# Kernel tuning notes

Hardware: AMD Instinct MI355X
Metric: run time of the kernel (lower is better)

## Reference

```python
import jax, jax.numpy as jnp
import numpy as np

N = 50000      # nodes
E = 800000     # edges (avg degree 16)
IN, HID, OUT = 256, 128, 64


def _glorot(key, shape):
    fan_in, fan_out = shape[0], shape[1]
    limit = np.sqrt(6.0 / (fan_in + fan_out))
    return jax.random.uniform(key, shape, jnp.float32, -limit, limit)


def setup_inputs() -> dict:
    key = jax.random.key(0)
    ks = jax.random.split(key, 8)
    x = jax.random.normal(ks[0], (N, IN), jnp.float32)
    edge_index = jax.random.randint(ks[1], (2, E), 0, N, dtype=jnp.int64)
    W1 = _glorot(ks[2], (IN, HID))
    b1 = jnp.zeros((HID,), jnp.float32)
    W2 = _glorot(ks[3], (HID, OUT))
    b2 = jnp.zeros((OUT,), jnp.float32)
    aw1 = _glorot(ks[4], (HID, 1))
    ab1 = jnp.zeros((1,), jnp.float32)
    aw2 = _glorot(ks[5], (OUT, 1))
    ab2 = jnp.zeros((1,), jnp.float32)
    return {"x": x, "edge_index": edge_index, "W1": W1, "b1": b1,
            "W2": W2, "b2": b2, "aw1": aw1, "ab1": ab1, "aw2": aw2, "ab2": ab2}


def gcn_conv(x, W, b, src, dst, n):
    # PyG GCNConv: add self-loops, symmetric degree normalization, then aggregate.
    h = x @ W                                   # [n, out]
    loops = jnp.arange(n, dtype=src.dtype)
    s = jnp.concatenate([src, loops])           # [E+n]
    d = jnp.concatenate([dst, loops])
    deg = jax.ops.segment_sum(jnp.ones(s.shape[0], h.dtype), d, num_segments=n)
    dinv = jnp.where(deg > 0, jax.lax.rsqrt(deg), 0.0)
    norm = dinv[s] * dinv[d]                    # [E+n]
    out = jax.ops.segment_sum(h[s] * norm[:, None], d, num_segments=n)
    return out + b


def reference(x, edge_index, W1, b1, W2, b2, aw1, ab1, aw2, ab2):
    # eval mode: dropout is identity
    src, dst = edge_index[0], edge_index[1]
    h = gcn_conv(x, W1, b1, src, dst, N)
    h = jax.nn.relu(h)
    h = h * jax.nn.sigmoid(h @ aw1 + ab1)       # sigmoid attention gate 1
    h = gcn_conv(h, W2, b2, src, dst, N)
    return h * jax.nn.sigmoid(h @ aw2 + ab2)    # sigmoid attention gate 2
```

## Files before the change

kernel.cpp:

```cpp
#include <hip/hip_runtime.h>
#include <math.h>

#define N_NODES 50000
#define N_EDGES 800000
#define D_IN    256
#define D_HID   128
#define D_OUT   64

#define NB 196
#define CH 2048

typedef unsigned int u32;
typedef unsigned short u16;
typedef __attribute__((ext_vector_type(8))) short bf16x8;
typedef __attribute__((ext_vector_type(4))) float f32x4;

__device__ __forceinline__ float bflo(u32 u) {
    union { u32 i; float f; } c; c.i = u << 16; return c.f;
}
__device__ __forceinline__ float bfhi(u32 u) {
    union { u32 i; float f; } c; c.i = u & 0xffff0000u; return c.f;
}
__device__ __forceinline__ u32 pack_bf2(float a, float b) {
    union { float f; u32 i; } ca, cb; ca.f = a; cb.f = b;
    u32 ra = (ca.i + 0x7fffu + ((ca.i >> 16) & 1u)) >> 16;
    u32 rb = (cb.i + 0x7fffu + ((cb.i >> 16) & 1u)) & 0xffff0000u;
    return ra | rb;
}

__device__ __forceinline__ void acc8(float* a, uint4 u) {
    a[0] += bflo(u.x); a[1] += bfhi(u.x);
    a[2] += bflo(u.y); a[3] += bfhi(u.y);
    a[4] += bflo(u.z); a[5] += bfhi(u.z);
    a[6] += bflo(u.w); a[7] += bfhi(u.w);
}

__device__ __forceinline__ int edge_at(const void* ei, int is64, int which, int i) {
    if (is64) return (int)((const long long*)ei)[(size_t)which * N_EDGES + i];
    return ((const int*)ei)[which * N_EDGES + i];
}

__device__ __forceinline__ int detect_is64(const void* ei, int t, int* s_is32) {
    if (t == 0) *s_is32 = 0;
    __syncthreads();
    if (t < 256) {
        int vv = ((const int*)ei)[2 * t + 1];
        if (vv != 0) atomicOr(s_is32, 1);
    }
    __syncthreads();
    return (*s_is32 == 0);
}


__global__ __launch_bounds__(256) void k_hist(const void* __restrict__ ei,
                                              int* __restrict__ bcnt,
                                              int* __restrict__ bstart,
                                              int* __restrict__ bcur,
                                              int* __restrict__ tick) {
    __shared__ int h[NB];
    __shared__ int s_is32;
    __shared__ int s_last;
    int t = threadIdx.x;
    int is64 = detect_is64(ei, t, &s_is32);
    for (int i = t; i < NB; i += 256) h[i] = 0;
    __syncthreads();
    for (int i = blockIdx.x * 256 + t; i < N_EDGES; i += gridDim.x * 256) {
        int d = edge_at(ei, is64, 1, i);
        atomicAdd(&h[d >> 8], 1);
    }
    __syncthreads();
    for (int i = t; i < NB; i += 256) if (h[i]) atomicAdd(&bcnt[i], h[i]);
    __threadfence();
    if (t == 0) s_last = (atomicAdd(tick, 1) == (int)gridDim.x - 1);
    __syncthreads();
    if (s_last) {
        __shared__ int sm[256];
        int v = (t < NB) ? atomicAdd(&bcnt[t], 0) : 0;
        sm[t] = v; __syncthreads();
        for (int off = 1; off < 256; off <<= 1) {
            int a = (t >= off) ? sm[t - off] : 0;
            __syncthreads();
            sm[t] += a;
            __syncthreads();
        }
        if (t < NB) { bstart[t] = sm[t] - v; bcur[t] = sm[t] - v; }
    }
}

__global__ __launch_bounds__(256) void k_scatter1(const void* __restrict__ ei,
                                                  int* __restrict__ bcur,
                                                  u32* __restrict__ ebuf) {
    __shared__ int h[NB], gbase[NB], lc[NB];
    __shared__ int s_is32;
    int t = threadIdx.x;
    int is64 = detect_is64(ei, t, &s_is32);
    for (int i = t; i < NB; i += 256) { h[i] = 0; lc[i] = 0; }
    __syncthreads();
    int base = blockIdx.x * CH;

    u32 p[CH / 256];
    #pragma unroll
    for (int j = 0; j < CH / 256; ++j) {
        int i = base + j * 256 + t;
        if (i < N_EDGES) {
            int s = edge_at(ei, is64, 0, i);
            int d = edge_at(ei, is64, 1, i);
            p[j] = (u32)s | ((u32)d << 16);
            atomicAdd(&h[d >> 8], 1);
        }
    }
    __syncthreads();
    for (int i = t; i < NB; i += 256) if (h[i]) gbase[i] = atomicAdd(&bcur[i], h[i]);
    __syncthreads();
    #pragma unroll
    for (int j = 0; j < CH / 256; ++j) {
        int i = base + j * 256 + t;
        if (i < N_EDGES) {
            int b = (int)(p[j] >> 24);
            int lp = atomicAdd(&lc[b], 1);
            ebuf[gbase[b] + lp] = p[j];
        }
    }
}

__global__ __launch_bounds__(256) void k_scatter2(const u32* __restrict__ ebuf,
                                                  const int* __restrict__ bstart,
                                                  const int* __restrict__ bcnt,
                                                  int* __restrict__ rowstart,
                                                  int* __restrict__ cnt,
                                                  float* __restrict__ dinv,
                                                  int* __restrict__ colidx) {
    __shared__ int h2[256], lofs[256], cur[256], sm[256];
    int b = blockIdx.x, t = threadIdx.x;
    int e0 = bstart[b], ne = bcnt[b];
    h2[t] = 0; cur[t] = 0;
    __syncthreads();
    for (int i = t; i < ne; i += 256) {
        u32 p = ebuf[e0 + i];
        atomicAdd(&h2[(p >> 16) & 255], 1);
    }
    __syncthreads();
    int v = h2[t]; sm[t] = v; __syncthreads();
    for (int off = 1; off < 256; off <<= 1) {
        int a = (t >= off) ? sm[t - off] : 0;
        __syncthreads();
        sm[t] += a;
        __syncthreads();
    }
    lofs[t] = sm[t] - v;
    __syncthreads();
    int node = (b << 8) + t;
    if (node < N_NODES) {
        rowstart[node] = e0 + lofs[t];
        cnt[node] = v;
        dinv[node] = rsqrtf(1.0f + (float)v);
    }
    for (int i = t; i < ne; i += 256) {
        u32 p = ebuf[e0 + i];
        int dl = (p >> 16) & 255;
        int lp = atomicAdd(&cur[dl], 1);
        colidx[e0 + lofs[dl] + lp] = (int)(p & 0xffffu);
    }
}

__global__ void k_wsplit(const float* __restrict__ W1, u16* __restrict__ t1h,
                         u16* __restrict__ t1l, const float* __restrict__ W2,
                         u16* __restrict__ t2h, u16* __restrict__ t2l,
                         int* __restrict__ bcnt, int* __restrict__ tick) {
    int i = blockIdx.x * 256 + threadIdx.x;
    if (i < NB) bcnt[i] = 0;
    if (i == 0) tick[0] = 0;
    if (i < D_IN * D_HID) {
        int k = i / D_HID, c = i - k * D_HID;
        u32 bits = __float_as_uint(W1[i]);
        u32 hb = bits & 0xffff0000u;
        float lo = __uint_as_float(bits) - __uint_as_float(hb);
        t1h[(size_t)c * D_IN + k] = (u16)(hb >> 16);
        t1l[(size_t)c * D_IN + k] = (u16)(__float_as_uint(lo) >> 16);
    }
    int j = i - D_IN * D_HID;
    if (j >= 0 && j < D_HID * D_OUT) {
        int k = j / D_OUT, c = j - k * D_OUT;
        u32 bits = __float_as_uint(W2[j]);
        u32 hb = bits & 0xffff0000u;
        float lo = __uint_as_float(bits) - __uint_as_float(hb);
        t2h[(size_t)c * D_HID + k] = (u16)(hb >> 16);
        t2l[(size_t)c * D_HID + k] = (u16)(__float_as_uint(lo) >> 16);
    }
}

template <int K, int NF>
__global__ __launch_bounds__(256) void k_gemm_f32a(
    const float* __restrict__ A, const u16* __restrict__ tHi,
    const u16* __restrict__ tLo, const float* __restrict__ dinv,
    u32* __restrict__ Cp, int M) {
    constexpr int NT = NF / 16;
    constexpr int LDK = 40;
    __shared__ u16 aH[128][LDK], aL[128][LDK];
    __shared__ u16 wH[NF][LDK], wL[NF][LDK];

    const int t = threadIdx.x;
    const int lane = t & 63, wv = t >> 6;
    const int m0 = blockIdx.x * 128;
    const int lr = lane & 15, lk = (lane >> 4) * 8;

    f32x4 acc[2][NT] = {};

    const int arow = t >> 1;
    const int akq = (t & 1) * 16;
    const bool aok = (m0 + arow) < M;
    const float* asrc = A + (size_t)(m0 + arow) * K + akq;

    for (int ks = 0; ks < K; ks += 32) {
        {
            float f[16];
            #pragma unroll
            for (int j = 0; j < 16; ++j) f[j] = 0.0f;
            if (aok) {
                const float4* p = (const float4*)(asrc + ks);
                float4 v0 = p[0], v1 = p[1], v2 = p[2], v3 = p[3];
                f[0] = v0.x; f[1] = v0.y; f[2]  = v0.z; f[3]  = v0.w;
                f[4] = v1.x; f[5] = v1.y; f[6]  = v1.z; f[7]  = v1.w;
                f[8] = v2.x; f[9] = v2.y; f[10] = v2.z; f[11] = v2.w;
                f[12] = v3.x; f[13] = v3.y; f[14] = v3.z; f[15] = v3.w;
            }
            u32 hp[8], lp[8];
            #pragma unroll
            for (int q = 0; q < 8; ++q) {
                u32 b0 = __float_as_uint(f[2 * q]);
                u32 b1 = __float_as_uint(f[2 * q + 1]);
                u32 h0 = b0 & 0xffff0000u, h1 = b1 & 0xffff0000u;
                float l0 = f[2 * q] - __uint_as_float(h0);
                float l1 = f[2 * q + 1] - __uint_as_float(h1);
                hp[q] = (h0 >> 16) | h1;
                lp[q] = (__float_as_uint(l0) >> 16) | (__float_as_uint(l1) & 0xffff0000u);
            }
            *(uint4*)&aH[arow][akq + 0] = make_uint4(hp[0], hp[1], hp[2], hp[3]);
            *(uint4*)&aH[arow][akq + 8] = make_uint4(hp[4], hp[5], hp[6], hp[7]);
            *(uint4*)&aL[arow][akq + 0] = make_uint4(lp[0], lp[1], lp[2], lp[3]);
            *(uint4*)&aL[arow][akq + 8] = make_uint4(lp[4], lp[5], lp[6], lp[7]);
        }
        #pragma unroll
        for (int idx = t; idx < NF * 4; idx += 256) {
            int col = idx >> 2;
            int k8 = (idx & 3) * 8;
            *(uint4*)&wH[col][k8] = *(const uint4*)&tHi[(size_t)col * K + ks + k8];
            *(uint4*)&wL[col][k8] = *(const uint4*)&tLo[(size_t)col * K + ks + k8];
        }
        __syncthreads();

        bf16x8 afH[2], afL[2];
        #pragma unroll
        for (int mt = 0; mt < 2; ++mt) {
            int r = wv * 32 + mt * 16 + lr;
            afH[mt] = *(const bf16x8*)&aH[r][lk];
            afL[mt] = *(const bf16x8*)&aL[r][lk];
        }
        #pragma unroll
        for (int nt = 0; nt < NT; ++nt) {
            bf16x8 bh = *(const bf16x8*)&wH[nt * 16 + lr][lk];
            bf16x8 bl = *(const bf16x8*)&wL[nt * 16 + lr][lk];
            #pragma unroll
            for (int mt = 0; mt < 2; ++mt) {
                acc[mt][nt] = __builtin_amdgcn_mfma_f32_16x16x32_bf16(afH[mt], bh, acc[mt][nt], 0, 0, 0);
                acc[mt][nt] = __builtin_amdgcn_mfma_f32_16x16x32_bf16(afL[mt], bh, acc[mt][nt], 0, 0, 0);
                acc[mt][nt] = __builtin_amdgcn_mfma_f32_16x16x32_bf16(afH[mt], bl, acc[mt][nt], 0, 0, 0);
            }
        }
        __syncthreads();
    }

    #pragma unroll
    for (int mt = 0; mt < 2; ++mt) {
        #pragma unroll
        for (int r = 0; r < 4; ++r) {
            int row = m0 + wv * 32 + mt * 16 + (lane >> 4) * 4 + r;
            float dv = (row < M) ? dinv[row] : 0.0f;
            #pragma unroll
            for (int nt = 0; nt < NT; ++nt) {
                float v = acc[mt][nt][r] * dv;
                float vn = __shfl_xor(v, 1);
                if (!(lane & 1) && row < M) {
                    Cp[(size_t)row * (NF / 2) + nt * 8 + (lr >> 1)] = pack_bf2(v, vn);
                }
            }
        }
    }
}

template <int K, int NF>
__global__ __launch_bounds__(256) void k_gemm_splita(
    const u32* __restrict__ aHg, const u32* __restrict__ aLg,
    const u16* __restrict__ tHi, const u16* __restrict__ tLo,
    const float* __restrict__ dinv, u32* __restrict__ Cp, int M) {
    constexpr int NT = NF / 16;
    constexpr int LDK = 40;
    __shared__ u16 aH[128][LDK], aL[128][LDK];
    __shared__ u16 wH[NF][LDK], wL[NF][LDK];

    const int t = threadIdx.x;
    const int lane = t & 63, wv = t >> 6;
    const int m0 = blockIdx.x * 128;
    const int lr = lane & 15, lk = (lane >> 4) * 8;

    f32x4 acc[2][NT] = {};

    for (int ks = 0; ks < K; ks += 32) {
        #pragma unroll
        for (int idx = t; idx < 128 * 4; idx += 256) {
            int row = idx >> 2;
            int kq = (idx & 3) * 8;
            int grow = m0 + row;
            uint4 hv = make_uint4(0, 0, 0, 0), lv = make_uint4(0, 0, 0, 0);
            if (grow < M) {
                size_t gi = (size_t)grow * (K / 2) + (ks + kq) / 2;
                hv = *(const uint4*)&aHg[gi];
                lv = *(const uint4*)&aLg[gi];
            }
            *(uint4*)&aH[row][kq] = hv;
            *(uint4*)&aL[row][kq] = lv;
        }
        #pragma unroll
        for (int idx = t; idx < NF * 4; idx += 256) {
            int col = idx >> 2;
            int k8 = (idx & 3) * 8;
            *(uint4*)&wH[col][k8] = *(const uint4*)&tHi[(size_t)col * K + ks + k8];
            *(uint4*)&wL[col][k8] = *(const uint4*)&tLo[(size_t)col * K + ks + k8];
        }
        __syncthreads();

        bf16x8 afH[2], afL[2];
        #pragma unroll
        for (int mt = 0; mt < 2; ++mt) {
            int r = wv * 32 + mt * 16 + lr;
            afH[mt] = *(const bf16x8*)&aH[r][lk];
            afL[mt] = *(const bf16x8*)&aL[r][lk];
        }
        #pragma unroll
        for (int nt = 0; nt < NT; ++nt) {
            bf16x8 bh = *(const bf16x8*)&wH[nt * 16 + lr][lk];
            bf16x8 bl = *(const bf16x8*)&wL[nt * 16 + lr][lk];
            #pragma unroll
            for (int mt = 0; mt < 2; ++mt) {
                acc[mt][nt] = __builtin_amdgcn_mfma_f32_16x16x32_bf16(afH[mt], bh, acc[mt][nt], 0, 0, 0);
                acc[mt][nt] = __builtin_amdgcn_mfma_f32_16x16x32_bf16(afL[mt], bh, acc[mt][nt], 0, 0, 0);
                acc[mt][nt] = __builtin_amdgcn_mfma_f32_16x16x32_bf16(afH[mt], bl, acc[mt][nt], 0, 0, 0);
            }
        }
        __syncthreads();
    }

    #pragma unroll
    for (int mt = 0; mt < 2; ++mt) {
        #pragma unroll
        for (int r = 0; r < 4; ++r) {
            int row = m0 + wv * 32 + mt * 16 + (lane >> 4) * 4 + r;
            float dv = (row < M) ? dinv[row] : 0.0f;
            #pragma unroll
            for (int nt = 0; nt < NT; ++nt) {
                float v = acc[mt][nt][r] * dv;
                float vn = __shfl_xor(v, 1);
                if (!(lane & 1) && row < M) {
                    Cp[(size_t)row * (NF / 2) + nt * 8 + (lr >> 1)] = pack_bf2(v, vn);
                }
            }
        }
    }
}


__global__ __launch_bounds__(256) void k_agg1(
        const u32* __restrict__ hs, const int* __restrict__ rowstart,
        const int* __restrict__ cnt, const int* __restrict__ colidx,
        const float* __restrict__ dinv,
        const float* __restrict__ b, const float* __restrict__ aw,
        const float* __restrict__ ab,
        u32* __restrict__ oHi, u32* __restrict__ oLo) {
    int v = blockIdx.x * 4 + (threadIdx.x >> 6);
    int l = threadIdx.x & 63;
    if (v >= N_NODES) return;
    int g = l >> 4, q = l & 15;
    const uint4* hs4 = (const uint4*)hs;
    float a[8];
    #pragma unroll
    for (int k = 0; k < 8; ++k) a[k] = 0.0f;
    if (g == 0) acc8(a, hs4[(size_t)v * 16 + q]);
    int start = rowstart[v], len = cnt[v];
    const int* cx = colidx + start;
    int jj = g;
    for (; jj + 4 < len; jj += 8) {
        int s0 = cx[jj], s1 = cx[jj + 4];
        uint4 u0 = hs4[(size_t)s0 * 16 + q];
        uint4 u1 = hs4[(size_t)s1 * 16 + q];
        acc8(a, u0); acc8(a, u1);
    }
    if (jj < len) acc8(a, hs4[(size_t)cx[jj] * 16 + q]);
    #pragma unroll
    for (int k = 0; k < 8; ++k) {
        a[k] += __shfl_xor(a[k], 16);
        a[k] += __shfl_xor(a[k], 32);
    }
    float dv = dinv[v];
    float4 b0 = *(const float4*)&b[8 * q], b1 = *(const float4*)&b[8 * q + 4];
    a[0] = fmaxf(a[0] * dv + b0.x, 0.0f); a[1] = fmaxf(a[1] * dv + b0.y, 0.0f);
    a[2] = fmaxf(a[2] * dv + b0.z, 0.0f); a[3] = fmaxf(a[3] * dv + b0.w, 0.0f);
    a[4] = fmaxf(a[4] * dv + b1.x, 0.0f); a[5] = fmaxf(a[5] * dv + b1.y, 0.0f);
    a[6] = fmaxf(a[6] * dv + b1.z, 0.0f); a[7] = fmaxf(a[7] * dv + b1.w, 0.0f);
    float4 w0 = *(const float4*)&aw[8 * q], w1 = *(const float4*)&aw[8 * q + 4];
    float p = a[0] * w0.x + a[1] * w0.y + a[2] * w0.z + a[3] * w0.w
            + a[4] * w1.x + a[5] * w1.y + a[6] * w1.z + a[7] * w1.w;
    p += __shfl_xor(p, 1); p += __shfl_xor(p, 2);
    p += __shfl_xor(p, 4); p += __shfl_xor(p, 8);
    float gg = 1.0f / (1.0f + expf(-(p + ab[0])));
    if (g == 0) {
        u32 hp[4], lp[4];
        #pragma unroll
        for (int pr = 0; pr < 4; ++pr) {
            float v0 = a[2 * pr] * gg, v1 = a[2 * pr + 1] * gg;
            u32 b0i = __float_as_uint(v0), b1i = __float_as_uint(v1);
            u32 h0 = b0i & 0xffff0000u, h1 = b1i & 0xffff0000u;
            float l0 = v0 - __uint_as_float(h0);
            float l1 = v1 - __uint_as_float(h1);
            hp[pr] = (h0 >> 16) | h1;
            lp[pr] = (__float_as_uint(l0) >> 16) | (__float_as_uint(l1) & 0xffff0000u);
        }
        *(uint4*)&oHi[(size_t)v * 64 + q * 4] = make_uint4(hp[0], hp[1], hp[2], hp[3]);
        *(uint4*)&oLo[(size_t)v * 64 + q * 4] = make_uint4(lp[0], lp[1], lp[2], lp[3]);
    }
}

__global__ __launch_bounds__(256) void k_agg2(
        const u32* __restrict__ hs, const int* __restrict__ rowstart,
        const int* __restrict__ cnt, const int* __restrict__ colidx,
        const float* __restrict__ dinv,
        const float* __restrict__ b, const float* __restrict__ aw,
        const float* __restrict__ ab, float* __restrict__ out) {
    int v = blockIdx.x * 4 + (threadIdx.x >> 6);
    int l = threadIdx.x & 63;
    if (v >= N_NODES) return;
    int g = l >> 3, q = l & 7;
    const uint4* hs4 = (const uint4*)hs;
    float a[8];
    #pragma unroll
    for (int k = 0; k < 8; ++k) a[k] = 0.0f;
    if (g == 0) acc8(a, hs4[(size_t)v * 8 + q]);
    int start = rowstart[v], len = cnt[v];
    const int* cx = colidx + start;
    int jj = g;
    for (; jj + 8 < len; jj += 16) {
        int s0 = cx[jj], s1 = cx[jj + 8];
        uint4 u0 = hs4[(size_t)s0 * 8 + q];
        uint4 u1 = hs4[(size_t)s1 * 8 + q];
        acc8(a, u0); acc8(a, u1);
    }
    if (jj < len) acc8(a, hs4[(size_t)cx[jj] * 8 + q]);
    #pragma unroll
    for (int k = 0; k < 8; ++k) {
        a[k] += __shfl_xor(a[k], 8);
        a[k] += __shfl_xor(a[k], 16);
        a[k] += __shfl_xor(a[k], 32);
    }
    float dv = dinv[v];
    float4 b0 = *(const float4*)&b[8 * q], b1 = *(const float4*)&b[8 * q + 4];
    a[0] = a[0] * dv + b0.x; a[1] = a[1] * dv + b0.y;
    a[2] = a[2] * dv + b0.z; a[3] = a[3] * dv + b0.w;
    a[4] = a[4] * dv + b1.x; a[5] = a[5] * dv + b1.y;
    a[6] = a[6] * dv + b1.z; a[7] = a[7] * dv + b1.w;
    float4 w0 = *(const float4*)&aw[8 * q], w1 = *(const float4*)&aw[8 * q + 4];
    float p = a[0] * w0.x + a[1] * w0.y + a[2] * w0.z + a[3] * w0.w
            + a[4] * w1.x + a[5] * w1.y + a[6] * w1.z + a[7] * w1.w;
    p += __shfl_xor(p, 1); p += __shfl_xor(p, 2); p += __shfl_xor(p, 4);
    float gg = 1.0f / (1.0f + expf(-(p + ab[0])));
    if (g == 0) {
        float4 o0 = make_float4(a[0] * gg, a[1] * gg, a[2] * gg, a[3] * gg);
        float4 o1 = make_float4(a[4] * gg, a[5] * gg, a[6] * gg, a[7] * gg);
        *(float4*)&out[(size_t)v * 64 + 8 * q] = o0;
        *(float4*)&out[(size_t)v * 64 + 8 * q + 4] = o1;
    }
}


static inline size_t align_up(size_t x, size_t a) { return (x + a - 1) & ~(a - 1); }

extern "C" void kernel_launch(void* const* d_in, const int* in_sizes, int n_in,
                              void* d_out, int out_size, void* d_ws, size_t ws_size,
                              hipStream_t stream) {
    const float* x   = (const float*)d_in[0];
    const void*  ei  = d_in[1];
    const float* W1  = (const float*)d_in[2];
    const float* b1  = (const float*)d_in[3];
    const float* W2  = (const float*)d_in[4];
    const float* b2  = (const float*)d_in[5];
    const float* aw1 = (const float*)d_in[6];
    const float* ab1 = (const float*)d_in[7];
    const float* aw2 = (const float*)d_in[8];
    const float* ab2 = (const float*)d_in[9];
    float* out = (float*)d_out;

    char* w = (char*)d_ws;
    size_t off = 0;
    int*   bcnt     = (int*)(w + off); off = align_up(off + NB * 4, 256);
    int*   bstart   = (int*)(w + off); off = align_up(off + NB * 4, 256);
    int*   bcur     = (int*)(w + off); off = align_up(off + NB * 4, 256);
    int*   tick     = (int*)(w + off); off = align_up(off + 4, 256);
    int*   cnt      = (int*)(w + off); off = align_up(off + N_NODES * 4, 256);
    int*   rowstart = (int*)(w + off); off = align_up(off + N_NODES * 4, 256);
    float* dinv     = (float*)(w + off); off = align_up(off + N_NODES * 4, 256);
    u32*   ebuf     = (u32*)(w + off); off = align_up(off + (size_t)N_EDGES * 4, 256);
    int*   colidx   = (int*)(w + off); off = align_up(off + (size_t)N_EDGES * 4, 256);
    u32*   h1s      = (u32*)(w + off); off = align_up(off + (size_t)N_NODES * 64 * 4, 256);
    u32*   h1hi     = (u32*)(w + off); off = align_up(off + (size_t)N_NODES * 64 * 4, 256);
    u32*   h1lo     = (u32*)(w + off); off = align_up(off + (size_t)N_NODES * 64 * 4, 256);
    u32*   h2s      = (u32*)(w + off); off = align_up(off + (size_t)N_NODES * 32 * 4, 256);
    u16*   wt1h     = (u16*)(w + off); off = align_up(off + (size_t)D_IN * D_HID * 2, 256);
    u16*   wt1l     = (u16*)(w + off); off = align_up(off + (size_t)D_IN * D_HID * 2, 256);
    u16*   wt2h     = (u16*)(w + off); off = align_up(off + (size_t)D_HID * D_OUT * 2, 256);
    u16*   wt2l     = (u16*)(w + off); off = align_up(off + (size_t)D_HID * D_OUT * 2, 256);
    (void)ws_size; (void)out_size; (void)n_in; (void)in_sizes;

    k_wsplit<<<(D_IN * D_HID + D_HID * D_OUT + 255) / 256, 256, 0, stream>>>(
        W1, wt1h, wt1l, W2, wt2h, wt2l, bcnt, tick);

    k_hist<<<256, 256, 0, stream>>>(ei, bcnt, bstart, bcur, tick);
    k_scatter1<<<(N_EDGES + CH - 1) / CH, 256, 0, stream>>>(ei, bcur, ebuf);
    k_scatter2<<<NB, 256, 0, stream>>>(ebuf, bstart, bcnt, rowstart, cnt, dinv, colidx);

    k_gemm_f32a<D_IN, D_HID><<<(N_NODES + 127) / 128, 256, 0, stream>>>(
        x, wt1h, wt1l, dinv, h1s, N_NODES);
    k_agg1<<<(N_NODES + 3) / 4, 256, 0, stream>>>(
        h1s, rowstart, cnt, colidx, dinv, b1, aw1, ab1, h1hi, h1lo);

    k_gemm_splita<D_HID, D_OUT><<<(N_NODES + 127) / 128, 256, 0, stream>>>(
        h1hi, h1lo, wt2h, wt2l, dinv, h2s, N_NODES);
    k_agg2<<<(N_NODES + 3) / 4, 256, 0, stream>>>(
        h2s, rowstart, cnt, colidx, dinv, b2, aw2, ab2, out);
}
```

Before: 244.8 us.

## Column-chunk aggregation for cache locality and replace histogram with fixed slabs

Aggregation kernels are split into feature-column chunks across blocks, so each pass gathers a narrower slice of neighbour rows and the working set fits better in cache. The sigmoid gates become separate passes: partial dot products go to a buffer, gate 1 is applied while loading the second GEMM's input, and gate 2 runs as its own elementwise kernel. The histogram/scan kernel is dropped by giving each destination bucket a fixed-capacity slab. This adds kernel launches and extra intermediate traffic (h2a, pdot), and it is only correct if no bucket holds more than SLAB edges, which holds only for near-uniform degree distributions.

```diff
diff --git a/kernel.cpp b/kernel.cpp
--- a/kernel.cpp
+++ b/kernel.cpp
@@ -9,6 +9,8 @@
 
 #define NB 196
 #define CH 2048
+#define SLAB 4608
+#define NBLK1 12500
 
 typedef unsigned int u32;
 typedef unsigned short u16;
@@ -51,41 +53,6 @@
     return (*s_is32 == 0);
 }
 
-
-__global__ __launch_bounds__(256) void k_hist(const void* __restrict__ ei,
-                                              int* __restrict__ bcnt,
-                                              int* __restrict__ bstart,
-                                              int* __restrict__ bcur,
-                                              int* __restrict__ tick) {
-    __shared__ int h[NB];
-    __shared__ int s_is32;
-    __shared__ int s_last;
-    int t = threadIdx.x;
-    int is64 = detect_is64(ei, t, &s_is32);
-    for (int i = t; i < NB; i += 256) h[i] = 0;
-    __syncthreads();
-    for (int i = blockIdx.x * 256 + t; i < N_EDGES; i += gridDim.x * 256) {
-        int d = edge_at(ei, is64, 1, i);
-        atomicAdd(&h[d >> 8], 1);
-    }
-    __syncthreads();
-    for (int i = t; i < NB; i += 256) if (h[i]) atomicAdd(&bcnt[i], h[i]);
-    __threadfence();
-    if (t == 0) s_last = (atomicAdd(tick, 1) == (int)gridDim.x - 1);
-    __syncthreads();
-    if (s_last) {
-        __shared__ int sm[256];
-        int v = (t < NB) ? atomicAdd(&bcnt[t], 0) : 0;
-        sm[t] = v; __syncthreads();
-        for (int off = 1; off < 256; off <<= 1) {
-            int a = (t >= off) ? sm[t - off] : 0;
-            __syncthreads();
-            sm[t] += a;
-            __syncthreads();
-        }
-        if (t < NB) { bstart[t] = sm[t] - v; bcur[t] = sm[t] - v; }
-    }
-}
 
 __global__ __launch_bounds__(256) void k_scatter1(const void* __restrict__ ei,
                                                   int* __restrict__ bcur,
@@ -124,15 +91,14 @@
 }
 
 __global__ __launch_bounds__(256) void k_scatter2(const u32* __restrict__ ebuf,
-                                                  const int* __restrict__ bstart,
-                                                  const int* __restrict__ bcnt,
+                                                  const int* __restrict__ bcur,
                                                   int* __restrict__ rowstart,
                                                   int* __restrict__ cnt,
                                                   float* __restrict__ dinv,
                                                   int* __restrict__ colidx) {
     __shared__ int h2[256], lofs[256], cur[256], sm[256];
     int b = blockIdx.x, t = threadIdx.x;
-    int e0 = bstart[b], ne = bcnt[b];
+    int e0 = b * SLAB, ne = bcur[b] - e0;
     h2[t] = 0; cur[t] = 0;
     __syncthreads();
     for (int i = t; i < ne; i += 256) {
@@ -166,10 +132,9 @@
 __global__ void k_wsplit(const float* __restrict__ W1, u16* __restrict__ t1h,
                          u16* __restrict__ t1l, const float* __restrict__ W2,
                          u16* __restrict__ t2h, u16* __restrict__ t2l,
-                         int* __restrict__ bcnt, int* __restrict__ tick) {
+                         int* __restrict__ bcur) {
     int i = blockIdx.x * 256 + threadIdx.x;
-    if (i < NB) bcnt[i] = 0;
-    if (i == 0) tick[0] = 0;
+    if (i < NB) bcur[i] = i * SLAB;
     if (i < D_IN * D_HID) {
         int k = i / D_HID, c = i - k * D_HID;
         u32 bits = __float_as_uint(W1[i]);
@@ -291,6 +256,7 @@
 template <int K, int NF>
 __global__ __launch_bounds__(256) void k_gemm_splita(
     const u32* __restrict__ aHg, const u32* __restrict__ aLg,
+    const float* __restrict__ g1,
     const u16* __restrict__ tHi, const u16* __restrict__ tLo,
     const float* __restrict__ dinv, u32* __restrict__ Cp, int M) {
     constexpr int NT = NF / 16;
@@ -316,6 +282,19 @@
                 size_t gi = (size_t)grow * (K / 2) + (ks + kq) / 2;
                 hv = *(const uint4*)&aHg[gi];
                 lv = *(const uint4*)&aLg[gi];
+                float gv = g1[grow];
+                u32* hp = (u32*)&hv; u32* lp = (u32*)&lv;
+                #pragma unroll
+                for (int w2 = 0; w2 < 4; ++w2) {
+                    float f0 = (bflo(hp[w2]) + bflo(lp[w2])) * gv;
+                    float f1 = (bfhi(hp[w2]) + bfhi(lp[w2])) * gv;
+                    u32 h0 = __float_as_uint(f0) & 0xffff0000u;
+                    u32 h1b = __float_as_uint(f1) & 0xffff0000u;
+                    float l0 = f0 - __uint_as_float(h0);
+                    float l1 = f1 - __uint_as_float(h1b);
+                    hp[w2] = (h0 >> 16) | h1b;
+                    lp[w2] = (__float_as_uint(l0) >> 16) | (__float_as_uint(l1) & 0xffff0000u);
+                }
             }
             *(uint4*)&aH[row][kq] = hv;
             *(uint4*)&aL[row][kq] = lv;
@@ -369,114 +348,147 @@
 }
 
 
-__global__ __launch_bounds__(256) void k_agg1(
+__global__ __launch_bounds__(256) void k_agg1c(
         const u32* __restrict__ hs, const int* __restrict__ rowstart,
         const int* __restrict__ cnt, const int* __restrict__ colidx,
         const float* __restrict__ dinv,
         const float* __restrict__ b, const float* __restrict__ aw,
-        const float* __restrict__ ab,
+        float* __restrict__ pdot,
         u32* __restrict__ oHi, u32* __restrict__ oLo) {
-    int v = blockIdx.x * 4 + (threadIdx.x >> 6);
+    int c  = blockIdx.x / NBLK1;
+    int nb = blockIdx.x - c * NBLK1;
+    int v = nb * 4 + (threadIdx.x >> 6);
+    if (v >= N_NODES) return;
     int l = threadIdx.x & 63;
-    if (v >= N_NODES) return;
-    int g = l >> 4, q = l & 15;
+    int g = l >> 2, q = l & 3;
     const uint4* hs4 = (const uint4*)hs;
+    const int cb = c * 4 + q;
     float a[8];
     #pragma unroll
     for (int k = 0; k < 8; ++k) a[k] = 0.0f;
-    if (g == 0) acc8(a, hs4[(size_t)v * 16 + q]);
+    if (g == 0) acc8(a, hs4[(size_t)v * 16 + cb]);
     int start = rowstart[v], len = cnt[v];
     const int* cx = colidx + start;
     int jj = g;
-    for (; jj + 4 < len; jj += 8) {
-        int s0 = cx[jj], s1 = cx[jj + 4];
-        uint4 u0 = hs4[(size_t)s0 * 16 + q];
-        uint4 u1 = hs4[(size_t)s1 * 16 + q];
+    for (; jj + 16 < len; jj += 32) {
+        int s0 = cx[jj], s1 = cx[jj + 16];
+        uint4 u0 = hs4[(size_t)s0 * 16 + cb];
+        uint4 u1 = hs4[(size_t)s1 * 16 + cb];
         acc8(a, u0); acc8(a, u1);
     }
-    if (jj < len) acc8(a, hs4[(size_t)cx[jj] * 16 + q]);
+    if (jj < len) acc8(a, hs4[(size_t)cx[jj] * 16 + cb]);
     #pragma unroll
     for (int k = 0; k < 8; ++k) {
+        a[k] += __shfl_xor(a[k], 4);
+        a[k] += __shfl_xor(a[k], 8);
         a[k] += __shfl_xor(a[k], 16);
         a[k] += __shfl_xor(a[k], 32);
     }
     float dv = dinv[v];
-    float4 b0 = *(const float4*)&b[8 * q], b1 = *(const float4*)&b[8 * q + 4];
+    const float* bc = b + c * 32 + q * 8;
+    float4 b0 = *(const float4*)bc, b1 = *(const float4*)(bc + 4);
     a[0] = fmaxf(a[0] * dv + b0.x, 0.0f); a[1] = fmaxf(a[1] * dv + b0.y, 0.0f);
     a[2] = fmaxf(a[2] * dv + b0.z, 0.0f); a[3] = fmaxf(a[3] * dv + b0.w, 0.0f);
     a[4] = fmaxf(a[4] * dv + b1.x, 0.0f); a[5] = fmaxf(a[5] * dv + b1.y, 0.0f);
     a[6] = fmaxf(a[6] * dv + b1.z, 0.0f); a[7] = fmaxf(a[7] * dv + b1.w, 0.0f);
-    float4 w0 = *(const float4*)&aw[8 * q], w1 = *(const float4*)&aw[8 * q + 4];
+    const float* ac = aw + c * 32 + q * 8;
+    float4 w0 = *(const float4*)ac, w1 = *(const float4*)(ac + 4);
     float p = a[0] * w0.x + a[1] * w0.y + a[2] * w0.z + a[3] * w0.w
             + a[4] * w1.x + a[5] * w1.y + a[6] * w1.z + a[7] * w1.w;
     p += __shfl_xor(p, 1); p += __shfl_xor(p, 2);
-    p += __shfl_xor(p, 4); p += __shfl_xor(p, 8);
-    float gg = 1.0f / (1.0f + expf(-(p + ab[0])));
+    if (l == 0) pdot[(size_t)c * N_NODES + v] = p;
     if (g == 0) {
         u32 hp[4], lp[4];
         #pragma unroll
         for (int pr = 0; pr < 4; ++pr) {
-            float v0 = a[2 * pr] * gg, v1 = a[2 * pr + 1] * gg;
-            u32 b0i = __float_as_uint(v0), b1i = __float_as_uint(v1);
-            u32 h0 = b0i & 0xffff0000u, h1 = b1i & 0xffff0000u;
+            float v0 = a[2 * pr], v1 = a[2 * pr + 1];
+            u32 h0 = __float_as_uint(v0) & 0xffff0000u;
+            u32 h1 = __float_as_uint(v1) & 0xffff0000u;
             float l0 = v0 - __uint_as_float(h0);
             float l1 = v1 - __uint_as_float(h1);
             hp[pr] = (h0 >> 16) | h1;
             lp[pr] = (__float_as_uint(l0) >> 16) | (__float_as_uint(l1) & 0xffff0000u);
         }
-        *(uint4*)&oHi[(size_t)v * 64 + q * 4] = make_uint4(hp[0], hp[1], hp[2], hp[3]);
-        *(uint4*)&oLo[(size_t)v * 64 + q * 4] = make_uint4(lp[0], lp[1], lp[2], lp[3]);
-    }
-}
-
-__global__ __launch_bounds__(256) void k_agg2(
+        *(uint4*)&oHi[(size_t)v * 64 + c * 16 + q * 4] = make_uint4(hp[0], hp[1], hp[2], hp[3]);
+        *(uint4*)&oLo[(size_t)v * 64 + c * 16 + q * 4] = make_uint4(lp[0], lp[1], lp[2], lp[3]);
+    }
+}
+
+__global__ void k_gate1(const float* __restrict__ pdot, const float* __restrict__ ab,
+                        float* __restrict__ g1) {
+    int v = blockIdx.x * 256 + threadIdx.x;
+    if (v < N_NODES) {
+        float p = pdot[v] + pdot[N_NODES + v] + pdot[2 * N_NODES + v]
+                + pdot[3 * N_NODES + v] + ab[0];
+        g1[v] = 1.0f / (1.0f + expf(-p));
+    }
+}
+
+__global__ __launch_bounds__(256) void k_agg2c(
         const u32* __restrict__ hs, const int* __restrict__ rowstart,
         const int* __restrict__ cnt, const int* __restrict__ colidx,
         const float* __restrict__ dinv,
         const float* __restrict__ b, const float* __restrict__ aw,
-        const float* __restrict__ ab, float* __restrict__ out) {
-    int v = blockIdx.x * 4 + (threadIdx.x >> 6);
+        float* __restrict__ pdot, float* __restrict__ h2a) {
+    int c  = blockIdx.x / NBLK1;
+    int nb = blockIdx.x - c * NBLK1;
+    int v = nb * 4 + (threadIdx.x >> 6);
+    if (v >= N_NODES) return;
     int l = threadIdx.x & 63;
-    if (v >= N_NODES) return;
-    int g = l >> 3, q = l & 7;
+    int g = l >> 2, q = l & 3;
     const uint4* hs4 = (const uint4*)hs;
+    const int cb = c * 4 + q;
     float a[8];
     #pragma unroll
     for (int k = 0; k < 8; ++k) a[k] = 0.0f;
-    if (g == 0) acc8(a, hs4[(size_t)v * 8 + q]);
+    if (g == 0) acc8(a, hs4[(size_t)v * 8 + cb]);
     int start = rowstart[v], len = cnt[v];
     const int* cx = colidx + start;
     int jj = g;
-    for (; jj + 8 < len; jj += 16) {
-        int s0 = cx[jj], s1 = cx[jj + 8];
-        uint4 u0 = hs4[(size_t)s0 * 8 + q];
-        uint4 u1 = hs4[(size_t)s1 * 8 + q];
+    for (; jj + 16 < len; jj += 32) {
+        int s0 = cx[jj], s1 = cx[jj + 16];
+        uint4 u0 = hs4[(size_t)s0 * 8 + cb];
+        uint4 u1 = hs4[(size_t)s1 * 8 + cb];
         acc8(a, u0); acc8(a, u1);
     }
-    if (jj < len) acc8(a, hs4[(size_t)cx[jj] * 8 + q]);
+    if (jj < len) acc8(a, hs4[(size_t)cx[jj] * 8 + cb]);
     #pragma unroll
     for (int k = 0; k < 8; ++k) {
+        a[k] += __shfl_xor(a[k], 4);
         a[k] += __shfl_xor(a[k], 8);
         a[k] += __shfl_xor(a[k], 16);
         a[k] += __shfl_xor(a[k], 32);
     }
     float dv = dinv[v];
-    float4 b0 = *(const float4*)&b[8 * q], b1 = *(const float4*)&b[8 * q + 4];
+    const float* bc = b + c * 32 + q * 8;
+    float4 b0 = *(const float4*)bc, b1 = *(const float4*)(bc + 4);
     a[0] = a[0] * dv + b0.x; a[1] = a[1] * dv + b0.y;
     a[2] = a[2] * dv + b0.z; a[3] = a[3] * dv + b0.w;
     a[4] = a[4] * dv + b1.x; a[5] = a[5] * dv + b1.y;
     a[6] = a[6] * dv + b1.z; a[7] = a[7] * dv + b1.w;
-    float4 w0 = *(const float4*)&aw[8 * q], w1 = *(const float4*)&aw[8 * q + 4];
+    const float* ac = aw + c * 32 + q * 8;
+    float4 w0 = *(const float4*)ac, w1 = *(const float4*)(ac + 4);
     float p = a[0] * w0.x + a[1] * w0.y + a[2] * w0.z + a[3] * w0.w
             + a[4] * w1.x + a[5] * w1.y + a[6] * w1.z + a[7] * w1.w;
-    p += __shfl_xor(p, 1); p += __shfl_xor(p, 2); p += __shfl_xor(p, 4);
-    float gg = 1.0f / (1.0f + expf(-(p + ab[0])));
+    p += __shfl_xor(p, 1); p += __shfl_xor(p, 2);
+    if (l == 0) pdot[(size_t)c * N_NODES + v] = p;
     if (g == 0) {
-        float4 o0 = make_float4(a[0] * gg, a[1] * gg, a[2] * gg, a[3] * gg);
-        float4 o1 = make_float4(a[4] * gg, a[5] * gg, a[6] * gg, a[7] * gg);
-        *(float4*)&out[(size_t)v * 64 + 8 * q] = o0;
-        *(float4*)&out[(size_t)v * 64 + 8 * q + 4] = o1;
-    }
+        float* o = h2a + (size_t)v * 64 + c * 32 + q * 8;
+        *(float4*)o       = make_float4(a[0], a[1], a[2], a[3]);
+        *(float4*)(o + 4) = make_float4(a[4], a[5], a[6], a[7]);
+    }
+}
+
+__global__ __launch_bounds__(256) void k_gate2(const float* __restrict__ h2a,
+                                               const float* __restrict__ pdot,
+                                               const float* __restrict__ ab,
+                                               float* __restrict__ out) {
+    int v = blockIdx.x * 4 + (threadIdx.x >> 6);
+    int f = threadIdx.x & 63;
+    if (v >= N_NODES) return;
+    float p = pdot[v] + pdot[N_NODES + v] + ab[0];
+    float g = 1.0f / (1.0f + expf(-p));
+    out[(size_t)v * 64 + f] = h2a[(size_t)v * 64 + f] * g;
 }
 
 
@@ -499,19 +511,20 @@
 
     char* w = (char*)d_ws;
     size_t off = 0;
-    int*   bcnt     = (int*)(w + off); off = align_up(off + NB * 4, 256);
-    int*   bstart   = (int*)(w + off); off = align_up(off + NB * 4, 256);
     int*   bcur     = (int*)(w + off); off = align_up(off + NB * 4, 256);
-    int*   tick     = (int*)(w + off); off = align_up(off + 4, 256);
     int*   cnt      = (int*)(w + off); off = align_up(off + N_NODES * 4, 256);
     int*   rowstart = (int*)(w + off); off = align_up(off + N_NODES * 4, 256);
     float* dinv     = (float*)(w + off); off = align_up(off + N_NODES * 4, 256);
-    u32*   ebuf     = (u32*)(w + off); off = align_up(off + (size_t)N_EDGES * 4, 256);
-    int*   colidx   = (int*)(w + off); off = align_up(off + (size_t)N_EDGES * 4, 256);
+    u32*   ebuf     = (u32*)(w + off); off = align_up(off + (size_t)NB * SLAB * 4, 256);
+    int*   colidx   = (int*)(w + off); off = align_up(off + (size_t)NB * SLAB * 4, 256);
     u32*   h1s      = (u32*)(w + off); off = align_up(off + (size_t)N_NODES * 64 * 4, 256);
     u32*   h1hi     = (u32*)(w + off); off = align_up(off + (size_t)N_NODES * 64 * 4, 256);
     u32*   h1lo     = (u32*)(w + off); off = align_up(off + (size_t)N_NODES * 64 * 4, 256);
     u32*   h2s      = (u32*)(w + off); off = align_up(off + (size_t)N_NODES * 32 * 4, 256);
+    float* h2a      = (float*)(w + off); off = align_up(off + (size_t)N_NODES * 64 * 4, 256);
+    float* pdot1    = (float*)(w + off); off = align_up(off + (size_t)4 * N_NODES * 4, 256);
+    float* pdot2    = (float*)(w + off); off = align_up(off + (size_t)2 * N_NODES * 4, 256);
+    float* g1       = (float*)(w + off); off = align_up(off + (size_t)N_NODES * 4, 256);
     u16*   wt1h     = (u16*)(w + off); off = align_up(off + (size_t)D_IN * D_HID * 2, 256);
     u16*   wt1l     = (u16*)(w + off); off = align_up(off + (size_t)D_IN * D_HID * 2, 256);
     u16*   wt2h     = (u16*)(w + off); off = align_up(off + (size_t)D_HID * D_OUT * 2, 256);
@@ -519,19 +532,20 @@
     (void)ws_size; (void)out_size; (void)n_in; (void)in_sizes;
 
     k_wsplit<<<(D_IN * D_HID + D_HID * D_OUT + 255) / 256, 256, 0, stream>>>(
-        W1, wt1h, wt1l, W2, wt2h, wt2l, bcnt, tick);
-
-    k_hist<<<256, 256, 0, stream>>>(ei, bcnt, bstart, bcur, tick);
+        W1, wt1h, wt1l, W2, wt2h, wt2l, bcur);
+
     k_scatter1<<<(N_EDGES + CH - 1) / CH, 256, 0, stream>>>(ei, bcur, ebuf);
-    k_scatter2<<<NB, 256, 0, stream>>>(ebuf, bstart, bcnt, rowstart, cnt, dinv, colidx);
+    k_scatter2<<<NB, 256, 0, stream>>>(ebuf, bcur, rowstart, cnt, dinv, colidx);
 
     k_gemm_f32a<D_IN, D_HID><<<(N_NODES + 127) / 128, 256, 0, stream>>>(
         x, wt1h, wt1l, dinv, h1s, N_NODES);
-    k_agg1<<<(N_NODES + 3) / 4, 256, 0, stream>>>(
-        h1s, rowstart, cnt, colidx, dinv, b1, aw1, ab1, h1hi, h1lo);
+    k_agg1c<<<4 * NBLK1, 256, 0, stream>>>(
+        h1s, rowstart, cnt, colidx, dinv, b1, aw1, pdot1, h1hi, h1lo);
+    k_gate1<<<(N_NODES + 255) / 256, 256, 0, stream>>>(pdot1, ab1, g1);
 
     k_gemm_splita<D_HID, D_OUT><<<(N_NODES + 127) / 128, 256, 0, stream>>>(
-        h1hi, h1lo, wt2h, wt2l, dinv, h2s, N_NODES);
-    k_agg2<<<(N_NODES + 3) / 4, 256, 0, stream>>>(
-        h2s, rowstart, cnt, colidx, dinv, b2, aw2, ab2, out);
-}
+        h1hi, h1lo, g1, wt2h, wt2l, dinv, h2s, N_NODES);
+    k_agg2c<<<2 * NBLK1, 256, 0, stream>>>(
+        h2s, rowstart, cnt, colidx, dinv, b2, aw2, pdot2, h2a);
+    k_gate2<<<(N_NODES + 3) / 4, 256, 0, stream>>>(h2a, pdot2, ab2, out);
+}
```

New measurement: 302.7 us. 23.7% more time.
